# Kernel optimization log

Hardware: AMD Instinct MI355X
Metric: run time of the kernel (lower is better)

## Reference

```python
import jax, jax.numpy as jnp
import numpy as np

DIM = 768
HEADS = 12
HD = DIM // HEADS
SCALE = float(np.sqrt(HD))  # sqrt(dim // num_heads)


def layernorm(x, g, b, eps=1e-5):
    m = jnp.mean(x, axis=-1, keepdims=True)
    v = jnp.var(x, axis=-1, keepdims=True)
    return (x - m) * jax.lax.rsqrt(v + eps) * g + b


def dwconv(x, w, b, pad):
    # x: [B,C,H,W], w: [C,1,kh,kw] depthwise
    y = jax.lax.conv_general_dilated(
        x, w, window_strides=(1, 1), padding=[(pad, pad), (pad, pad)],
        feature_group_count=x.shape[1], dimension_numbers=('NCHW', 'OIHW', 'NCHW'))
    return y + b[None, :, None, None]


def mha(xq, xkv, wq, bq, wk, bk, wv, bv, wo, bo):
    # per-head Linears batched over heads; wq/wk/wv: [H, C, hd], biases [H, hd]
    B, N, C = xq.shape
    q = jnp.einsum('bnc,hcd->bhnd', xq, wq) + bq[None, :, None, :]
    k = jnp.einsum('bnc,hcd->bhnd', xkv, wk) + bk[None, :, None, :]
    v = jnp.einsum('bnc,hcd->bhnd', xkv, wv) + bv[None, :, None, :]
    z = jax.nn.sigmoid(jnp.einsum('bhnd,bhmd->bhnm', q, k) / SCALE)  # sigmoid, not softmax
    o = jnp.einsum('bhnm,bhmd->bhnd', z, v)
    o = o.transpose(0, 2, 1, 3).reshape(B, N, C)  # concat heads along feature dim
    return o @ wo + bo


def reference(decoder, wq1, bq1, wk1, bk1, wv1, bv1, wo1, bo1,
              wq2, bq2, wk2, bk2, wv2, bv2, wo2, bo2,
              alphas1, alphas2, peg_w, peg_b,
              ln1_g, ln1_b, ln2_g, ln2_b,
              cn_dw_w, cn_dw_b, cn_ln_g, cn_ln_b,
              cn_w1, cn_b1, cn_w2, cn_b2, cn_scale, cn_alphas):
    B, C, H, W = decoder.shape
    x = decoder.transpose(0, 2, 3, 1).reshape(B, H * W, C)  # [B,N,C]
    # block 1: alpha * x + MHA(x,x,x)
    x = alphas1 * x + mha(x, x, wq1, bq1, wk1, bk1, wv1, bv1, wo1, bo1)
    # PEG: depthwise 3x3 conv (replaces x, no residual in source)
    x4 = x.reshape(B, H, W, C).transpose(0, 3, 1, 2)
    x4 = dwconv(x4, peg_w, peg_b, pad=1)
    x = x4.transpose(0, 2, 3, 1).reshape(B, H * W, C)
    x = layernorm(x, ln1_g, ln1_b)
    # block 2 (encoder is None -> self-attention)
    x = alphas2 * x + mha(x, x, wq2, bq2, wk2, bk2, wv2, bv2, wo2, bo2)
    x = layernorm(x, ln2_g, ln2_b)
    x4 = x.reshape(B, H, W, C).transpose(0, 3, 1, 2)  # [B,C,H,W]
    # CNBlock head: dwconv7x7 -> LN -> Linear(4d) -> GELU -> Linear(d), layer_scale + alpha residual
    y = dwconv(x4, cn_dw_w, cn_dw_b, pad=3)
    y = y.transpose(0, 2, 3, 1)  # [B,H,W,C]
    y = layernorm(y, cn_ln_g, cn_ln_b)
    y = jax.nn.gelu(y @ cn_w1 + cn_b1, approximate=False)
    y = y @ cn_w2 + cn_b2
    y = y.transpose(0, 3, 1, 2)  # [B,C,H,W]
    out = cn_scale[None, :, None, None] * y + x4 * cn_alphas[None, :, None, None]
    return out


def setup_inputs() -> dict:
    key = jax.random.key(0)
    ks = iter(jax.random.split(key, 40))
    def n(shape, s=0.02):
        return jax.random.normal(next(ks), shape, dtype=jnp.float32) * s
    d = {}
    d['decoder'] = jax.random.normal(next(ks), (8, DIM, 32, 32), dtype=jnp.float32)
    for i in (1, 2):
        d[f'wq{i}'] = n((HEADS, DIM, HD)); d[f'bq{i}'] = n((HEADS, HD), 1e-6)
        d[f'wk{i}'] = n((HEADS, DIM, HD)); d[f'bk{i}'] = n((HEADS, HD), 1e-6)
        d[f'wv{i}'] = n((HEADS, DIM, HD)); d[f'bv{i}'] = n((HEADS, HD), 1e-6)
        d[f'wo{i}'] = n((DIM, DIM)); d[f'bo{i}'] = n((DIM,), 1e-6)
    d['alphas1'] = jnp.ones((DIM,), jnp.float32)
    d['alphas2'] = jnp.ones((DIM,), jnp.float32)
    d['peg_w'] = n((DIM, 1, 3, 3), 0.1); d['peg_b'] = n((DIM,), 1e-6)
    d['ln1_g'] = jnp.ones((DIM,), jnp.float32); d['ln1_b'] = jnp.zeros((DIM,), jnp.float32)
    d['ln2_g'] = jnp.ones((DIM,), jnp.float32); d['ln2_b'] = jnp.zeros((DIM,), jnp.float32)
    d['cn_dw_w'] = n((DIM, 1, 7, 7), 0.1); d['cn_dw_b'] = n((DIM,), 0.02)
    d['cn_ln_g'] = jnp.ones((DIM,), jnp.float32); d['cn_ln_b'] = jnp.zeros((DIM,), jnp.float32)
    d['cn_w1'] = n((DIM, 4 * DIM)); d['cn_b1'] = n((4 * DIM,), 0.02)
    d['cn_w2'] = n((4 * DIM, DIM)); d['cn_b2'] = n((DIM,), 0.02)
    d['cn_scale'] = jnp.full((DIM,), 1e-6, jnp.float32)
    d['cn_alphas'] = jnp.ones((DIM,), jnp.float32)
    return d
```

## Files before the change

### kernel.cpp

```cpp
#include <hip/hip_runtime.h>
#include <math.h>

#define BATCH 8
#define CDIM 768
#define NTOK 1024
#define NH 12
#define HDIM 64

typedef __attribute__((ext_vector_type(8))) short bf16x8;
typedef __attribute__((ext_vector_type(4))) float f32x4;

__device__ inline short f2bf(float f) {
    union { float f; unsigned u; } v; v.f = f;
    unsigned r = (v.u + 0x7FFF + ((v.u >> 16) & 1)) >> 16;
    return (short)r;
}

__device__ inline void async_copy16(const short* g, short* l) {
    __builtin_amdgcn_global_load_lds(
        (const __attribute__((address_space(1))) void*)g,
        (__attribute__((address_space(3))) void*)l, 16, 0, 0);
}

__global__ void k_transpose_in(const float* __restrict__ dec, float* __restrict__ x,
                               short* __restrict__ xb) {
    __shared__ float tile[32][33];
    int b = blockIdx.z;
    int n0 = blockIdx.x * 32;
    int c0 = blockIdx.y * 32;
    int tx = threadIdx.x, ty = threadIdx.y;
#pragma unroll
    for (int r = 0; r < 4; ++r) {
        int c = c0 + ty + r * 8;
        tile[ty + r * 8][tx] = dec[((size_t)b * CDIM + c) * NTOK + n0 + tx];
    }
    __syncthreads();
#pragma unroll
    for (int r = 0; r < 4; ++r) {
        int n = n0 + ty + r * 8;
        float val = tile[tx][ty + r * 8];
        size_t idx = ((size_t)b * NTOK + n) * CDIM + c0 + tx;
        x[idx] = val;
        xb[idx] = f2bf(val);
    }
}

__global__ void k_wtrans(const float* __restrict__ src, short* __restrict__ dst,
                         int R, int C) {
    __shared__ float tile[32][33];
    int c0 = blockIdx.x * 32, r0 = blockIdx.y * 32;
    int tx = threadIdx.x, ty = threadIdx.y;
#pragma unroll
    for (int p = 0; p < 4; ++p)
        tile[ty + p * 8][tx] = src[(size_t)(r0 + ty + p * 8) * C + c0 + tx];
    __syncthreads();
#pragma unroll
    for (int p = 0; p < 4; ++p)
        dst[(size_t)(c0 + ty + p * 8) * R + r0 + tx] = f2bf(tile[tx][ty + p * 8]);
}

__global__ __launch_bounds__(256) void k_packqkv(
    const float* __restrict__ wq1, const float* __restrict__ wk1, const float* __restrict__ wv1,
    const float* __restrict__ wq2, const float* __restrict__ wk2, const float* __restrict__ wv2,
    short* __restrict__ dst1, short* __restrict__ dst2) {
    __shared__ float tile[64][65];
    int z = blockIdx.y;
    int set = z / 36, rem = z % 36, sect = rem / 12, h = rem % 12;
    const float* srcs[6] = {wq1, wk1, wv1, wq2, wk2, wv2};
    const float* src = srcs[set * 3 + sect] + (size_t)h * 768 * 64;
    short* dst = (set ? dst2 : dst1) + ((size_t)sect * 768 + h * 64) * 768;
    int k0 = blockIdx.x * 64;
    int t = threadIdx.x;
#pragma unroll
    for (int p = 0; p < 16; ++p) {
        int gid = t + p * 256;
        int r = gid >> 6, c = gid & 63;
        tile[r][c] = src[(size_t)(k0 + r) * 64 + c];
    }
    __syncthreads();
#pragma unroll
    for (int p = 0; p < 16; ++p) {
        int gid = t + p * 256;
        int d = gid >> 6, kk = gid & 63;
        dst[(size_t)d * 768 + k0 + kk] = f2bf(tile[kk][d]);
    }
}

__global__ void k_packbias(const float* __restrict__ bq1, const float* __restrict__ bk1,
                           const float* __restrict__ bv1, const float* __restrict__ bq2,
                           const float* __restrict__ bk2, const float* __restrict__ bv2,
                           float* __restrict__ d1, float* __restrict__ d2) {
    int tid = blockIdx.x * 256 + threadIdx.x;
    if (tid >= 4608) return;
    int set = tid / 2304, n = tid % 2304;
    int sect = n / 768, rem = n % 768;
    const float* srcs[6] = {bq1, bk1, bv1, bq2, bk2, bv2};
    float v = srcs[set * 3 + sect][rem];
    (set ? d2 : d1)[n] = v;
}

#define GM_FINAL 0
#define GM_PROJ  1
#define GM_GELU  2
#define GM_QKV   3
#define QKVSEC ((size_t)BATCH * NH * NTOK * HDIM)

template<int MODE, int BN>
__global__ __launch_bounds__(256) void k_gemm_mfma(
    const short* __restrict__ A, const short* __restrict__ Bt,
    const float* __restrict__ bias, const float* __restrict__ resid,
    const float* __restrict__ rscale, const float* __restrict__ alph,
    float* __restrict__ outF, short* __restrict__ outB, int M, int N, int K) {
    constexpr int NT = BN / 32;
    constexpr int BP = BN / 64;
    constexpr int STAGE = 2 * 128 * 32 + 2 * BN * 32;
    constexpr int FINALS = (MODE == GM_FINAL) ? 64 * 132 * 2 : 0;
    constexpr int SMEM = STAGE > FINALS ? STAGE : FINALS;
    __shared__ short smem[SMEM];
    short* As = smem;
    short* Bs = smem + 2 * 128 * 32;
    int t = threadIdx.x;
    int w = t >> 6, lane = t & 63, l15 = lane & 15, quad = lane >> 4;
    int r0 = blockIdx.x * 128, n0 = blockIdx.y * BN;
    int wr = (w >> 1) * 64, wc = (w & 1) * (BN / 2);
    f32x4 acc[4][NT];
#pragma unroll
    for (int i = 0; i < 4; ++i)
#pragma unroll
        for (int j = 0; j < NT; ++j) acc[i][j] = (f32x4){0.f, 0.f, 0.f, 0.f};
    int sr = t >> 2, sc = (t & 3) * 8;
    const short* Ag = A + (size_t)(r0 + sr) * K + sc;
    const short* Bg = Bt + (size_t)(n0 + sr) * K + sc;
    short* AsW = As + w * 512;
    short* BsW = Bs + w * 512;
#pragma unroll
    for (int p = 0; p < 2; ++p)
        async_copy16(Ag, AsW + p * 2048), Ag += (size_t)64 * K * 0;
#pragma unroll
    for (int p = 0; p < 2; ++p)
        ;
#pragma unroll
    for (int p = 0; p < 2; ++p)
        async_copy16(Ag + (size_t)p * 64 * K, AsW + p * 2048);
#pragma unroll
    for (int p = 0; p < BP; ++p)
        async_copy16(Bg + (size_t)p * 64 * K, BsW + p * 2048);
    int st = 0;
    for (int k0 = 0; k0 < K; k0 += 32, st ^= 1) {
        __syncthreads();
        if (k0 + 32 < K) {
            int nst = st ^ 1;
#pragma unroll
            for (int p = 0; p < 2; ++p)
                async_copy16(Ag + k0 + 32 + (size_t)p * 64 * K,
                             AsW + nst * 4096 + p * 2048);
#pragma unroll
            for (int p = 0; p < BP; ++p)
                async_copy16(Bg + k0 + 32 + (size_t)p * 64 * K,
                             BsW + nst * (BN * 32) + p * 2048);
        }
        bf16x8 af[4], bf[NT];
#pragma unroll
        for (int i = 0; i < 4; ++i)
            af[i] = *(const bf16x8*)&As[st * 4096 + (wr + i * 16 + l15) * 32 + quad * 8];
#pragma unroll
        for (int j = 0; j < NT; ++j)
            bf[j] = *(const bf16x8*)&Bs[st * (BN * 32) + (wc + j * 16 + l15) * 32 + quad * 8];
#pragma unroll
        for (int i = 0; i < 4; ++i)
#pragma unroll
            for (int j = 0; j < NT; ++j)
                acc[i][j] = __builtin_amdgcn_mfma_f32_16x16x32_bf16(af[i], bf[j], acc[i][j], 0, 0, 0);
    }
    if (MODE == GM_FINAL) {
        __syncthreads();
        float* T = (float*)smem;
#pragma unroll
        for (int i = 0; i < 4; ++i)
#pragma unroll
            for (int j = 0; j < NT; ++j)
#pragma unroll
                for (int rr = 0; rr < 4; ++rr) {
                    int rl = wr + i * 16 + quad * 4 + rr;
                    int cl = wc + j * 16 + l15;
                    int row = r0 + rl, col = n0 + cl;
                    float val = acc[i][j][rr] + bias[col];
                    val = rscale[col] * val + alph[col] * resid[(size_t)row * N + col];
                    T[cl * 132 + rl] = val;
                }
        __syncthreads();
        int c = t >> 2, qo = (t & 3) * 32;
        int b = r0 >> 10, tokbase = r0 & 1023;
        float* obase = outF + ((size_t)(b * 768 + n0 + c)) * 1024 + tokbase + qo;
#pragma unroll
        for (int ii = 0; ii < 8; ++ii)
            *(float4*)&obase[ii * 4] = *(float4*)&T[c * 132 + qo + ii * 4];
        return;
    }
#pragma unroll
    for (int i = 0; i < 4; ++i)
#pragma unroll
        for (int j = 0; j < NT; ++j)
#pragma unroll
            for (int rr = 0; rr < 4; ++rr) {
                int row = r0 + wr + i * 16 + quad * 4 + rr;
                int col = n0 + wc + j * 16 + l15;
                float val = acc[i][j][rr] + bias[col];
                if (MODE == GM_PROJ) {
                    val += rscale[col] * resid[(size_t)row * N + col];
                    outF[(size_t)row * N + col] = val;
                } else if (MODE == GM_GELU) {
                    float u = val * (1.0f + 0.044715f * val * val);
                    float zz = __builtin_amdgcn_rcpf(
                        1.0f + __builtin_amdgcn_exp2f(-2.3022082f * u));
                    outB[(size_t)row * N + col] = f2bf(val * zz);
                } else {
                    int sect = col / 768, rem = col - sect * 768;
                    int hh = rem >> 6, d = rem & 63;
                    int bb = row >> 10, tok = row & 1023;
                    outB[(size_t)sect * QKVSEC +
                         (((size_t)bb * NH + hh) * NTOK + tok) * HDIM + d] = f2bf(val);
                }
            }
}

__global__ __launch_bounds__(256) void k_attn_mfma(
    const short* __restrict__ q, const short* __restrict__ k,
    const short* __restrict__ v, short* __restrict__ o) {
    __shared__ short Ks[64][72];
    __shared__ short Vt[64][72];
    __shared__ short Ps[128][72];
    int b = blockIdx.z, h = blockIdx.y;
    int q0 = blockIdx.x * 128;
    int t = threadIdx.x;
    int w = t >> 6, lane = t & 63, l15 = lane & 15, quad = lane >> 4;
    size_t base = ((size_t)(b * NH + h)) * NTOK * HDIM;
    const short* qp = q + base;
    const short* kp = k + base;
    const short* vp = v + base;
    bf16x8 qf[2][2];
#pragma unroll
    for (int mt = 0; mt < 2; ++mt)
#pragma unroll
        for (int kc = 0; kc < 2; ++kc)
            qf[mt][kc] = *(const bf16x8*)&qp[(size_t)(q0 + w * 32 + mt * 16 + l15) * HDIM + kc * 32 + quad * 8];
    f32x4 oacc[2][4];
#pragma unroll
    for (int mt = 0; mt < 2; ++mt)
#pragma unroll
        for (int dt = 0; dt < 4; ++dt) oacc[mt][dt] = (f32x4){0.f, 0.f, 0.f, 0.f};
    for (int kt = 0; kt < 16; ++kt) {
        __syncthreads();
#pragma unroll
        for (int p = 0; p < 2; ++p) {
            int gid = t + p * 256;
            int r = gid >> 3, c8 = (gid & 7) * 8;
            *(bf16x8*)&Ks[r][c8] = *(const bf16x8*)&kp[(size_t)(kt * 64 + r) * HDIM + c8];
        }
#pragma unroll
        for (int p = 0; p < 2; ++p) {
            int tok = t & 63, d0 = (t >> 6) * 8 + p * 32;
            bf16x8 vv = *(const bf16x8*)&vp[(size_t)(kt * 64 + tok) * HDIM + d0];
#pragma unroll
            for (int j = 0; j < 8; ++j) Vt[d0 + j][tok] = vv[j];
        }
        __syncthreads();
        f32x4 sacc[2][4];
#pragma unroll
        for (int mt = 0; mt < 2; ++mt)
#pragma unroll
            for (int nt = 0; nt < 4; ++nt) sacc[mt][nt] = (f32x4){0.f, 0.f, 0.f, 0.f};
#pragma unroll
        for (int nt = 0; nt < 4; ++nt) {
            bf16x8 kf0 = *(const bf16x8*)&Ks[nt * 16 + l15][quad * 8];
            bf16x8 kf1 = *(const bf16x8*)&Ks[nt * 16 + l15][32 + quad * 8];
#pragma unroll
            for (int mt = 0; mt < 2; ++mt) {
                sacc[mt][nt] = __builtin_amdgcn_mfma_f32_16x16x32_bf16(qf[mt][0], kf0, sacc[mt][nt], 0, 0, 0);
                sacc[mt][nt] = __builtin_amdgcn_mfma_f32_16x16x32_bf16(qf[mt][1], kf1, sacc[mt][nt], 0, 0, 0);
            }
        }
#pragma unroll
        for (int mt = 0; mt < 2; ++mt)
#pragma unroll
            for (int nt = 0; nt < 4; ++nt)
#pragma unroll
                for (int rr = 0; rr < 4; ++rr) {
                    float s = sacc[mt][nt][rr];
                    float z = __builtin_amdgcn_rcpf(
                        1.0f + __builtin_amdgcn_exp2f(s * -0.18033688011112042f));
                    Ps[w * 32 + mt * 16 + quad * 4 + rr][nt * 16 + l15] = f2bf(z);
                }
        __syncthreads();
        bf16x8 vfr[2][4];
#pragma unroll
        for (int kc = 0; kc < 2; ++kc)
#pragma unroll
            for (int dt = 0; dt < 4; ++dt)
                vfr[kc][dt] = *(const bf16x8*)&Vt[dt * 16 + l15][kc * 32 + quad * 8];
#pragma unroll
        for (int mt = 0; mt < 2; ++mt)
#pragma unroll
            for (int kc = 0; kc < 2; ++kc) {
                bf16x8 pf = *(const bf16x8*)&Ps[w * 32 + mt * 16 + l15][kc * 32 + quad * 8];
#pragma unroll
                for (int dt = 0; dt < 4; ++dt)
                    oacc[mt][dt] = __builtin_amdgcn_mfma_f32_16x16x32_bf16(pf, vfr[kc][dt], oacc[mt][dt], 0, 0, 0);
            }
    }
#pragma unroll
    for (int mt = 0; mt < 2; ++mt)
#pragma unroll
        for (int dt = 0; dt < 4; ++dt)
#pragma unroll
            for (int rr = 0; rr < 4; ++rr) {
                int tok = q0 + w * 32 + mt * 16 + quad * 4 + rr;
                int c = h * 64 + dt * 16 + l15;
                o[((size_t)b * NTOK + tok) * CDIM + c] = f2bf(oacc[mt][dt][rr]);
            }
}

template<int K>
__global__ __launch_bounds__(256) void k_dwconv_t(
    const float* __restrict__ in, const float* __restrict__ w,
    const float* __restrict__ bias, float* __restrict__ out) {
    constexpr int PAD = K / 2;
    constexpr int KK = K * K;
    int t = threadIdx.x;
    int c = blockIdx.y * 64 + (t & 63);
    int j = blockIdx.x * 4 + (t >> 6);
    int b = blockIdx.z;
    float wr[KK];
#pragma unroll
    for (int qq = 0; qq < KK; ++qq) wr[qq] = w[(size_t)c * KK + qq];
    float bsv = bias[c];
    const float* base = in + (size_t)b * NTOK * CDIM + c;
    float win[K][K];
#pragma unroll
    for (int s = 1; s < K; ++s) {
        int ii = s - 1 - PAD;
#pragma unroll
        for (int qq = 0; qq < K; ++qq) {
            int jj = j - PAD + qq;
            win[s][qq] = (ii >= 0 && jj >= 0 && jj < 32)
                         ? base[(size_t)(ii * 32 + jj) * CDIM] : 0.0f;
        }
    }
#pragma unroll
    for (int i = 0; i < 32; ++i) {
#pragma unroll
        for (int r = 0; r < K - 1; ++r)
#pragma unroll
            for (int qq = 0; qq < K; ++qq) win[r][qq] = win[r + 1][qq];
        int ii = i + PAD;
#pragma unroll
        for (int qq = 0; qq < K; ++qq) {
            int jj = j - PAD + qq;
            win[K - 1][qq] = (ii < 32 && jj >= 0 && jj < 32)
                             ? base[(size_t)(ii * 32 + jj) * CDIM] : 0.0f;
        }
        float acc = bsv;
#pragma unroll
        for (int r = 0; r < K; ++r)
#pragma unroll
            for (int qq = 0; qq < K; ++qq)
                acc = fmaf(win[r][qq], wr[r * K + qq], acc);
        out[((size_t)b * NTOK + i * 32 + j) * CDIM + c] = acc;
    }
}

__global__ __launch_bounds__(256) void k_ln(
    const float* __restrict__ in, const float* __restrict__ g,
    const float* __restrict__ b, float* __restrict__ outF, short* __restrict__ outB) {
    int row = blockIdx.x;
    const float* xr = in + (size_t)row * CDIM;
    int t = threadIdx.x;
    float x0 = xr[t], x1 = xr[t + 256], x2 = xr[t + 512];
    float s = x0 + x1 + x2;
    float sq = x0 * x0 + x1 * x1 + x2 * x2;
#pragma unroll
    for (int off = 32; off > 0; off >>= 1) {
        s += __shfl_down(s, off);
        sq += __shfl_down(sq, off);
    }
    __shared__ float ws[4], wq2[4];
    int wid = t >> 6, lane = t & 63;
    if (lane == 0) { ws[wid] = s; wq2[wid] = sq; }
    __syncthreads();
    if (t == 0) {
        float S = ws[0] + ws[1] + ws[2] + ws[3];
        float Q = wq2[0] + wq2[1] + wq2[2] + wq2[3];
        float m = S * (1.0f / CDIM);
        float var = Q * (1.0f / CDIM) - m * m;
        ws[0] = m;
        wq2[0] = rsqrtf(var + 1e-5f);
    }
    __syncthreads();
    float m = ws[0], inv = wq2[0];
    float y0 = (x0 - m) * inv * g[t] + b[t];
    float y1 = (x1 - m) * inv * g[t + 256] + b[t + 256];
    float y2 = (x2 - m) * inv * g[t + 512] + b[t + 512];
    if (outF) {
        float* orow = outF + (size_t)row * CDIM;
        orow[t] = y0; orow[t + 256] = y1; orow[t + 512] = y2;
    }
    if (outB) {
        short* orow = outB + (size_t)row * CDIM;
        orow[t] = f2bf(y0); orow[t + 256] = f2bf(y1); orow[t + 512] = f2bf(y2);
    }
}

extern "C" void kernel_launch(void* const* d_in, const int* in_sizes, int n_in,
                              void* d_out, int out_size, void* d_ws, size_t ws_size,
                              hipStream_t stream) {
    const float* dec = (const float*)d_in[0];
    const float* wq1 = (const float*)d_in[1]; const float* bq1 = (const float*)d_in[2];
    const float* wk1 = (const float*)d_in[3]; const float* bk1 = (const float*)d_in[4];
    const float* wv1 = (const float*)d_in[5]; const float* bv1 = (const float*)d_in[6];
    const float* wo1 = (const float*)d_in[7]; const float* bo1 = (const float*)d_in[8];
    const float* wq2 = (const float*)d_in[9]; const float* bq2 = (const float*)d_in[10];
    const float* wk2 = (const float*)d_in[11]; const float* bk2 = (const float*)d_in[12];
    const float* wv2 = (const float*)d_in[13]; const float* bv2 = (const float*)d_in[14];
    const float* wo2 = (const float*)d_in[15]; const float* bo2 = (const float*)d_in[16];
    const float* alphas1 = (const float*)d_in[17];
    const float* alphas2 = (const float*)d_in[18];
    const float* peg_w = (const float*)d_in[19]; const float* peg_b = (const float*)d_in[20];
    const float* ln1_g = (const float*)d_in[21]; const float* ln1_b = (const float*)d_in[22];
    const float* ln2_g = (const float*)d_in[23]; const float* ln2_b = (const float*)d_in[24];
    const float* cn_dw_w = (const float*)d_in[25]; const float* cn_dw_b = (const float*)d_in[26];
    const float* cn_ln_g = (const float*)d_in[27]; const float* cn_ln_b = (const float*)d_in[28];
    const float* cn_w1 = (const float*)d_in[29]; const float* cn_b1 = (const float*)d_in[30];
    const float* cn_w2 = (const float*)d_in[31]; const float* cn_b2 = (const float*)d_in[32];
    const float* cn_scale = (const float*)d_in[33]; const float* cn_alphas = (const float*)d_in[34];
    float* out = (float*)d_out;

    const size_t S = (size_t)BATCH * NTOK * CDIM;
    float* A0 = (float*)d_ws;
    float* A1 = A0 + S;
    short* Xb  = (short*)(A1 + S);
    short* QKV = Xb + S;
    short* Ob  = QKV + 3 * S;
    short* Hb  = Ob + S;
    short* Wqkv1 = Hb + 2 * S;
    short* Wqkv2 = Wqkv1 + 2304 * 768;
    short* WoT1  = Wqkv2 + 2304 * 768;
    short* WoT2  = WoT1 + 768 * 768;
    short* W1T   = WoT2 + 768 * 768;
    short* W2T   = W1T + (size_t)3072 * 768;
    float* bqkv1 = (float*)(W2T + (size_t)768 * 3072);
    float* bqkv2 = bqkv1 + 2304;
    short* Hfull = QKV + 2 * S;

    dim3 tb(32, 8);
    dim3 dwgrid(8, 12, 8);

    k_packqkv<<<dim3(12, 72), 256, 0, stream>>>(wq1, wk1, wv1, wq2, wk2, wv2, Wqkv1, Wqkv2);
    k_wtrans<<<dim3(24, 24), tb, 0, stream>>>(wo1, WoT1, 768, 768);
    k_wtrans<<<dim3(24, 24), tb, 0, stream>>>(wo2, WoT2, 768, 768);
    k_wtrans<<<dim3(96, 24), tb, 0, stream>>>(cn_w1, W1T, 768, 3072);
    k_wtrans<<<dim3(24, 96), tb, 0, stream>>>(cn_w2, W2T, 3072, 768);
    k_packbias<<<18, 256, 0, stream>>>(bq1, bk1, bv1, bq2, bk2, bv2, bqkv1, bqkv2);

    k_transpose_in<<<dim3(32, 24, 8), tb, 0, stream>>>(dec, A0, Xb);

    k_gemm_mfma<GM_QKV, 128><<<dim3(64, 18), 256, 0, stream>>>(
        Xb, Wqkv1, bqkv1, nullptr, nullptr, nullptr, nullptr, QKV, 8192, 2304, 768);
    k_attn_mfma<<<dim3(8, 12, 8), 256, 0, stream>>>(QKV, QKV + S, QKV + 2 * S, Ob);
    k_gemm_mfma<GM_PROJ, 64><<<dim3(64, 12), 256, 0, stream>>>(
        Ob, WoT1, bo1, A0, alphas1, nullptr, A1, nullptr, 8192, 768, 768);
    k_dwconv_t<3><<<dwgrid, 256, 0, stream>>>(A1, peg_w, peg_b, A0);
    k_ln<<<8192, 256, 0, stream>>>(A0, ln1_g, ln1_b, A1, Xb);

    k_gemm_mfma<GM_QKV, 128><<<dim3(64, 18), 256, 0, stream>>>(
        Xb, Wqkv2, bqkv2, nullptr, nullptr, nullptr, nullptr, QKV, 8192, 2304, 768);
    k_attn_mfma<<<dim3(8, 12, 8), 256, 0, stream>>>(QKV, QKV + S, QKV + 2 * S, Ob);
    k_gemm_mfma<GM_PROJ, 64><<<dim3(64, 12), 256, 0, stream>>>(
        Ob, WoT2, bo2, A1, alphas2, nullptr, A0, nullptr, 8192, 768, 768);
    k_ln<<<8192, 256, 0, stream>>>(A0, ln2_g, ln2_b, A1, nullptr);

    k_dwconv_t<7><<<dwgrid, 256, 0, stream>>>(A1, cn_dw_w, cn_dw_b, A0);
    k_ln<<<8192, 256, 0, stream>>>(A0, cn_ln_g, cn_ln_b, nullptr, Xb);
    k_gemm_mfma<GM_GELU, 128><<<dim3(64, 24), 256, 0, stream>>>(
        Xb, W1T, cn_b1, nullptr, nullptr, nullptr, nullptr, Hfull, 8192, 3072, 768);
    k_gemm_mfma<GM_FINAL, 64><<<dim3(64, 12), 256, 0, stream>>>(
        Hfull, W2T, cn_b2, A1, cn_scale, cn_alphas, out, nullptr, 8192, 768, 3072);
}
```

Before: 619.4 us.

## Merge prep kernels into one launch and double-buffer the attention kernel

Seven weight-packing, bias-packing and input-transpose launches are folded into a single k_prep kernel that picks its task from the block index, which cuts launch overhead. The attention kernel now double-buffers K (async copied into a swizzled LDS layout) and V, swaps the MFMA operand order, writes P and the output as packed bf16 pairs, raises wave priority around the MFMA loops, and remaps blocks so that one XCD handles a contiguous set of heads. It also drops a stray duplicate async copy in the GEMM prologue. The cost is more LDS per attention block, a launch-bounds occupancy hint, and more complex control flow.

Result: faster. 578.6 us (-6.6%).

```diff
diff --git a/kernel.cpp b/kernel.cpp
--- a/kernel.cpp
+++ b/kernel.cpp
@@ -16,87 +16,95 @@
     return (short)r;
 }
 
+__device__ inline unsigned pack2bf(float lo, float hi) {
+    return (unsigned)(unsigned short)f2bf(lo) | ((unsigned)(unsigned short)f2bf(hi) << 16);
+}
+
 __device__ inline void async_copy16(const short* g, short* l) {
     __builtin_amdgcn_global_load_lds(
         (const __attribute__((address_space(1))) void*)g,
         (__attribute__((address_space(3))) void*)l, 16, 0, 0);
 }
 
-__global__ void k_transpose_in(const float* __restrict__ dec, float* __restrict__ x,
-                               short* __restrict__ xb) {
-    __shared__ float tile[32][33];
-    int b = blockIdx.z;
-    int n0 = blockIdx.x * 32;
-    int c0 = blockIdx.y * 32;
-    int tx = threadIdx.x, ty = threadIdx.y;
-#pragma unroll
-    for (int r = 0; r < 4; ++r) {
-        int c = c0 + ty + r * 8;
-        tile[ty + r * 8][tx] = dec[((size_t)b * CDIM + c) * NTOK + n0 + tx];
-    }
-    __syncthreads();
-#pragma unroll
-    for (int r = 0; r < 4; ++r) {
-        int n = n0 + ty + r * 8;
-        float val = tile[tx][ty + r * 8];
-        size_t idx = ((size_t)b * NTOK + n) * CDIM + c0 + tx;
-        x[idx] = val;
-        xb[idx] = f2bf(val);
-    }
-}
-
-__global__ void k_wtrans(const float* __restrict__ src, short* __restrict__ dst,
-                         int R, int C) {
-    __shared__ float tile[32][33];
-    int c0 = blockIdx.x * 32, r0 = blockIdx.y * 32;
-    int tx = threadIdx.x, ty = threadIdx.y;
-#pragma unroll
-    for (int p = 0; p < 4; ++p)
-        tile[ty + p * 8][tx] = src[(size_t)(r0 + ty + p * 8) * C + c0 + tx];
-    __syncthreads();
-#pragma unroll
-    for (int p = 0; p < 4; ++p)
-        dst[(size_t)(c0 + ty + p * 8) * R + r0 + tx] = f2bf(tile[tx][ty + p * 8]);
-}
-
-__global__ __launch_bounds__(256) void k_packqkv(
+__global__ __launch_bounds__(256) void k_prep(
     const float* __restrict__ wq1, const float* __restrict__ wk1, const float* __restrict__ wv1,
     const float* __restrict__ wq2, const float* __restrict__ wk2, const float* __restrict__ wv2,
-    short* __restrict__ dst1, short* __restrict__ dst2) {
-    __shared__ float tile[64][65];
-    int z = blockIdx.y;
-    int set = z / 36, rem = z % 36, sect = rem / 12, h = rem % 12;
-    const float* srcs[6] = {wq1, wk1, wv1, wq2, wk2, wv2};
-    const float* src = srcs[set * 3 + sect] + (size_t)h * 768 * 64;
-    short* dst = (set ? dst2 : dst1) + ((size_t)sect * 768 + h * 64) * 768;
-    int k0 = blockIdx.x * 64;
+    const float* __restrict__ wo1, const float* __restrict__ wo2,
+    const float* __restrict__ cnw1, const float* __restrict__ cnw2,
+    const float* __restrict__ bq1, const float* __restrict__ bk1, const float* __restrict__ bv1,
+    const float* __restrict__ bq2, const float* __restrict__ bk2, const float* __restrict__ bv2,
+    const float* __restrict__ dec,
+    short* __restrict__ Wqkv1, short* __restrict__ Wqkv2,
+    short* __restrict__ WoT1, short* __restrict__ WoT2,
+    short* __restrict__ W1T, short* __restrict__ W2T,
+    float* __restrict__ bqkv1, float* __restrict__ bqkv2,
+    float* __restrict__ A0, short* __restrict__ Xb) {
+    __shared__ float sh[64 * 65];
+    int bid = blockIdx.x;
     int t = threadIdx.x;
-#pragma unroll
-    for (int p = 0; p < 16; ++p) {
-        int gid = t + p * 256;
-        int r = gid >> 6, c = gid & 63;
-        tile[r][c] = src[(size_t)(k0 + r) * 64 + c];
-    }
-    __syncthreads();
-#pragma unroll
-    for (int p = 0; p < 16; ++p) {
-        int gid = t + p * 256;
-        int d = gid >> 6, kk = gid & 63;
-        dst[(size_t)d * 768 + k0 + kk] = f2bf(tile[kk][d]);
-    }
-}
-
-__global__ void k_packbias(const float* __restrict__ bq1, const float* __restrict__ bk1,
-                           const float* __restrict__ bv1, const float* __restrict__ bq2,
-                           const float* __restrict__ bk2, const float* __restrict__ bv2,
-                           float* __restrict__ d1, float* __restrict__ d2) {
-    int tid = blockIdx.x * 256 + threadIdx.x;
-    if (tid >= 4608) return;
-    int set = tid / 2304, n = tid % 2304;
-    int sect = n / 768, rem = n % 768;
-    const float* srcs[6] = {bq1, bk1, bv1, bq2, bk2, bv2};
-    float v = srcs[set * 3 + sect][rem];
-    (set ? d2 : d1)[n] = v;
+    if (bid < 864) {
+        int bx = bid % 12, z = bid / 12;
+        int set = z / 36, rem = z % 36, sect = rem / 12, hh = rem % 12;
+        const float* srcs[6] = {wq1, wk1, wv1, wq2, wk2, wv2};
+        const float* src = srcs[set * 3 + sect] + (size_t)hh * 768 * 64;
+        short* dst = (set ? Wqkv2 : Wqkv1) + ((size_t)sect * 768 + hh * 64) * 768;
+        int k0 = bx * 64;
+#pragma unroll
+        for (int p = 0; p < 16; ++p) {
+            int gid = t + p * 256;
+            int r = gid >> 6, c = gid & 63;
+            sh[r * 65 + c] = src[(size_t)(k0 + r) * 64 + c];
+        }
+        __syncthreads();
+#pragma unroll
+        for (int p = 0; p < 16; ++p) {
+            int gid = t + p * 256;
+            int d = gid >> 6, kk = gid & 63;
+            dst[(size_t)d * 768 + k0 + kk] = f2bf(sh[kk * 65 + d]);
+        }
+    } else if (bid < 6624) {
+        int r = bid - 864;
+        const float* src; short* dst; int R, C, bx, by;
+        if (r < 576)       { src = wo1;  dst = WoT1; R = 768;  C = 768;  bx = r % 24; by = r / 24; }
+        else if (r < 1152) { int s = r - 576;  src = wo2;  dst = WoT2; R = 768;  C = 768;  bx = s % 24; by = s / 24; }
+        else if (r < 3456) { int s = r - 1152; src = cnw1; dst = W1T;  R = 768;  C = 3072; bx = s % 96; by = s / 96; }
+        else               { int s = r - 3456; src = cnw2; dst = W2T;  R = 3072; C = 768;  bx = s % 24; by = s / 24; }
+        int c0 = bx * 32, r0 = by * 32, tx = t & 31, ty = t >> 5;
+#pragma unroll
+        for (int p = 0; p < 4; ++p)
+            sh[(ty + p * 8) * 33 + tx] = src[(size_t)(r0 + ty + p * 8) * C + c0 + tx];
+        __syncthreads();
+#pragma unroll
+        for (int p = 0; p < 4; ++p)
+            dst[(size_t)(c0 + ty + p * 8) * R + r0 + tx] = f2bf(sh[tx * 33 + ty + p * 8]);
+    } else if (bid < 6642) {
+        int tid = (bid - 6624) * 256 + t;
+        if (tid < 4608) {
+            int set = tid / 2304, n = tid % 2304;
+            int sect = n / 768, rem = n % 768;
+            const float* srcs[6] = {bq1, bk1, bv1, bq2, bk2, bv2};
+            float v = srcs[set * 3 + sect][rem];
+            (set ? bqkv2 : bqkv1)[n] = v;
+        }
+    } else {
+        int r = bid - 6642;
+        int bx = r % 32, by = (r / 32) % 24, bz = r / 768;
+        int n0 = bx * 32, c0 = by * 32, tx = t & 31, ty = t >> 5;
+#pragma unroll
+        for (int p = 0; p < 4; ++p) {
+            int c = c0 + ty + p * 8;
+            sh[(ty + p * 8) * 33 + tx] = dec[((size_t)bz * CDIM + c) * NTOK + n0 + tx];
+        }
+        __syncthreads();
+#pragma unroll
+        for (int p = 0; p < 4; ++p) {
+            int n = n0 + ty + p * 8;
+            float val = sh[tx * 33 + ty + p * 8];
+            size_t idx = ((size_t)bz * NTOK + n) * CDIM + c0 + tx;
+            A0[idx] = val;
+            Xb[idx] = f2bf(val);
+        }
+    }
 }
 
 #define GM_FINAL 0
@@ -133,12 +141,6 @@
     const short* Bg = Bt + (size_t)(n0 + sr) * K + sc;
     short* AsW = As + w * 512;
     short* BsW = Bs + w * 512;
-#pragma unroll
-    for (int p = 0; p < 2; ++p)
-        async_copy16(Ag, AsW + p * 2048), Ag += (size_t)64 * K * 0;
-#pragma unroll
-    for (int p = 0; p < 2; ++p)
-        ;
 #pragma unroll
     for (int p = 0; p < 2; ++p)
         async_copy16(Ag + (size_t)p * 64 * K, AsW + p * 2048);
@@ -224,100 +226,135 @@
             }
 }
 
-__global__ __launch_bounds__(256) void k_attn_mfma(
+__global__ __launch_bounds__(256, 3) void k_attn_mfma(
     const short* __restrict__ q, const short* __restrict__ k,
     const short* __restrict__ v, short* __restrict__ o) {
-    __shared__ short Ks[64][72];
-    __shared__ short Vt[64][72];
+    __shared__ short Ks[2][64 * 64];
+    __shared__ short Vt[2][64][72];
     __shared__ short Ps[128][72];
-    int b = blockIdx.z, h = blockIdx.y;
-    int q0 = blockIdx.x * 128;
     int t = threadIdx.x;
     int w = t >> 6, lane = t & 63, l15 = lane & 15, quad = lane >> 4;
+    int flat = blockIdx.x + (blockIdx.y << 3) + blockIdx.z * 96;
+    int xcd = flat & 7, slot = flat >> 3;
+    int qb = slot & 7, grp = xcd * 12 + (slot >> 3);
+    int h = grp % 12, b = grp / 12;
+    int q0 = qb * 128;
     size_t base = ((size_t)(b * NH + h)) * NTOK * HDIM;
     const short* qp = q + base;
     const short* kp = k + base;
     const short* vp = v + base;
+
     bf16x8 qf[2][2];
 #pragma unroll
-    for (int mt = 0; mt < 2; ++mt)
+    for (int nq = 0; nq < 2; ++nq)
 #pragma unroll
         for (int kc = 0; kc < 2; ++kc)
-            qf[mt][kc] = *(const bf16x8*)&qp[(size_t)(q0 + w * 32 + mt * 16 + l15) * HDIM + kc * 32 + quad * 8];
-    f32x4 oacc[2][4];
-#pragma unroll
-    for (int mt = 0; mt < 2; ++mt)
-#pragma unroll
-        for (int dt = 0; dt < 4; ++dt) oacc[mt][dt] = (f32x4){0.f, 0.f, 0.f, 0.f};
+            qf[nq][kc] = *(const bf16x8*)&qp[(size_t)(q0 + w * 32 + nq * 16 + l15) * HDIM + kc * 32 + quad * 8];
+
+    int r8 = lane >> 3;
+    const short* kg = kp + r8 * HDIM + (((lane & 7) ^ r8) << 3);
+    int vtok = t & 63, vd0 = (t >> 6) * 8;
+
+    f32x4 oacc[4][2];
+#pragma unroll
+    for (int dt = 0; dt < 4; ++dt)
+#pragma unroll
+        for (int nq = 0; nq < 2; ++nq) oacc[dt][nq] = (f32x4){0.f, 0.f, 0.f, 0.f};
+
+#pragma unroll
+    for (int p = 0; p < 2; ++p)
+        async_copy16(kg + (size_t)(p * 32 + w * 8) * HDIM, &Ks[0][(p * 32 + w * 8) * 64]);
+    {
+        bf16x8 v0 = *(const bf16x8*)&vp[(size_t)vtok * HDIM + vd0];
+        bf16x8 v1 = *(const bf16x8*)&vp[(size_t)vtok * HDIM + vd0 + 32];
+#pragma unroll
+        for (int j = 0; j < 8; ++j) {
+            Vt[0][vd0 + j][vtok] = v0[j];
+            Vt[0][vd0 + 32 + j][vtok] = v1[j];
+        }
+    }
+
+    short* prow0 = &Ps[w * 32 + l15][0];
+    short* prow1 = &Ps[w * 32 + 16 + l15][0];
+
     for (int kt = 0; kt < 16; ++kt) {
-        __syncthreads();
-#pragma unroll
-        for (int p = 0; p < 2; ++p) {
-            int gid = t + p * 256;
-            int r = gid >> 3, c8 = (gid & 7) * 8;
-            *(bf16x8*)&Ks[r][c8] = *(const bf16x8*)&kp[(size_t)(kt * 64 + r) * HDIM + c8];
-        }
-#pragma unroll
-        for (int p = 0; p < 2; ++p) {
-            int tok = t & 63, d0 = (t >> 6) * 8 + p * 32;
-            bf16x8 vv = *(const bf16x8*)&vp[(size_t)(kt * 64 + tok) * HDIM + d0];
-#pragma unroll
-            for (int j = 0; j < 8; ++j) Vt[d0 + j][tok] = vv[j];
-        }
-        __syncthreads();
-        f32x4 sacc[2][4];
-#pragma unroll
-        for (int mt = 0; mt < 2; ++mt)
-#pragma unroll
-            for (int nt = 0; nt < 4; ++nt) sacc[mt][nt] = (f32x4){0.f, 0.f, 0.f, 0.f};
-#pragma unroll
-        for (int nt = 0; nt < 4; ++nt) {
-            bf16x8 kf0 = *(const bf16x8*)&Ks[nt * 16 + l15][quad * 8];
-            bf16x8 kf1 = *(const bf16x8*)&Ks[nt * 16 + l15][32 + quad * 8];
-#pragma unroll
-            for (int mt = 0; mt < 2; ++mt) {
-                sacc[mt][nt] = __builtin_amdgcn_mfma_f32_16x16x32_bf16(qf[mt][0], kf0, sacc[mt][nt], 0, 0, 0);
-                sacc[mt][nt] = __builtin_amdgcn_mfma_f32_16x16x32_bf16(qf[mt][1], kf1, sacc[mt][nt], 0, 0, 0);
+        int cur = kt & 1, nxt = cur ^ 1;
+        __syncthreads();
+        bf16x8 vv0, vv1;
+        if (kt < 15) {
+            const short* kgn = kg + (size_t)((kt + 1) * 64) * HDIM;
+#pragma unroll
+            for (int p = 0; p < 2; ++p)
+                async_copy16(kgn + (size_t)(p * 32 + w * 8) * HDIM, &Ks[nxt][(p * 32 + w * 8) * 64]);
+            vv0 = *(const bf16x8*)&vp[((size_t)(kt + 1) * 64 + vtok) * HDIM + vd0];
+            vv1 = *(const bf16x8*)&vp[((size_t)(kt + 1) * 64 + vtok) * HDIM + vd0 + 32];
+        }
+        f32x4 sacc[4][2];
+#pragma unroll
+        for (int mk = 0; mk < 4; ++mk)
+#pragma unroll
+            for (int nq = 0; nq < 2; ++nq) sacc[mk][nq] = (f32x4){0.f, 0.f, 0.f, 0.f};
+        __builtin_amdgcn_s_setprio(1);
+#pragma unroll
+        for (int mk = 0; mk < 4; ++mk)
+#pragma unroll
+            for (int kc = 0; kc < 2; ++kc) {
+                bf16x8 kf = *(const bf16x8*)&Ks[cur][(mk * 16 + l15) * 64 + (((kc * 4 + quad) ^ (l15 & 7)) << 3)];
+#pragma unroll
+                for (int nq = 0; nq < 2; ++nq)
+                    sacc[mk][nq] = __builtin_amdgcn_mfma_f32_16x16x32_bf16(kf, qf[nq][kc], sacc[mk][nq], 0, 0, 0);
             }
-        }
-#pragma unroll
-        for (int mt = 0; mt < 2; ++mt)
-#pragma unroll
-            for (int nt = 0; nt < 4; ++nt)
-#pragma unroll
-                for (int rr = 0; rr < 4; ++rr) {
-                    float s = sacc[mt][nt][rr];
-                    float z = __builtin_amdgcn_rcpf(
-                        1.0f + __builtin_amdgcn_exp2f(s * -0.18033688011112042f));
-                    Ps[w * 32 + mt * 16 + quad * 4 + rr][nt * 16 + l15] = f2bf(z);
-                }
-        __syncthreads();
-        bf16x8 vfr[2][4];
+        __builtin_amdgcn_s_setprio(0);
+#pragma unroll
+        for (int mk = 0; mk < 4; ++mk)
+#pragma unroll
+            for (int nq = 0; nq < 2; ++nq) {
+                float z[4];
+#pragma unroll
+                for (int rr = 0; rr < 4; ++rr)
+                    z[rr] = __builtin_amdgcn_rcpf(
+                        1.0f + __builtin_amdgcn_exp2f(sacc[mk][nq][rr] * -0.18033688011112042f));
+                unsigned* pw = (unsigned*)((nq ? prow1 : prow0) + mk * 16 + quad * 4);
+                pw[0] = pack2bf(z[0], z[1]);
+                pw[1] = pack2bf(z[2], z[3]);
+            }
+        if (kt < 15) {
+#pragma unroll
+            for (int j = 0; j < 8; ++j) {
+                Vt[nxt][vd0 + j][vtok] = vv0[j];
+                Vt[nxt][vd0 + 32 + j][vtok] = vv1[j];
+            }
+        }
+        asm volatile("s_waitcnt lgkmcnt(0)" ::: "memory");
+        __builtin_amdgcn_sched_barrier(0);
+        bf16x8 pf[2][2];
 #pragma unroll
         for (int kc = 0; kc < 2; ++kc)
 #pragma unroll
-            for (int dt = 0; dt < 4; ++dt)
-                vfr[kc][dt] = *(const bf16x8*)&Vt[dt * 16 + l15][kc * 32 + quad * 8];
-#pragma unroll
-        for (int mt = 0; mt < 2; ++mt)
+            for (int nq = 0; nq < 2; ++nq)
+                pf[kc][nq] = *(const bf16x8*)((nq ? prow1 : prow0) + kc * 32 + quad * 8);
+        __builtin_amdgcn_s_setprio(1);
+#pragma unroll
+        for (int dt = 0; dt < 4; ++dt)
 #pragma unroll
             for (int kc = 0; kc < 2; ++kc) {
-                bf16x8 pf = *(const bf16x8*)&Ps[w * 32 + mt * 16 + l15][kc * 32 + quad * 8];
-#pragma unroll
-                for (int dt = 0; dt < 4; ++dt)
-                    oacc[mt][dt] = __builtin_amdgcn_mfma_f32_16x16x32_bf16(pf, vfr[kc][dt], oacc[mt][dt], 0, 0, 0);
+                bf16x8 vf = *(const bf16x8*)&Vt[cur][dt * 16 + l15][kc * 32 + quad * 8];
+#pragma unroll
+                for (int nq = 0; nq < 2; ++nq)
+                    oacc[dt][nq] = __builtin_amdgcn_mfma_f32_16x16x32_bf16(vf, pf[kc][nq], oacc[dt][nq], 0, 0, 0);
             }
-    }
-#pragma unroll
-    for (int mt = 0; mt < 2; ++mt)
-#pragma unroll
-        for (int dt = 0; dt < 4; ++dt)
-#pragma unroll
-            for (int rr = 0; rr < 4; ++rr) {
-                int tok = q0 + w * 32 + mt * 16 + quad * 4 + rr;
-                int c = h * 64 + dt * 16 + l15;
-                o[((size_t)b * NTOK + tok) * CDIM + c] = f2bf(oacc[mt][dt][rr]);
-            }
+        __builtin_amdgcn_s_setprio(0);
+    }
+#pragma unroll
+    for (int dt = 0; dt < 4; ++dt)
+#pragma unroll
+        for (int nq = 0; nq < 2; ++nq) {
+            int tok = q0 + w * 32 + nq * 16 + l15;
+            int c = h * 64 + dt * 16 + quad * 4;
+            unsigned* op = (unsigned*)&o[((size_t)b * NTOK + tok) * CDIM + c];
+            op[0] = pack2bf(oacc[dt][nq][0], oacc[dt][nq][1]);
+            op[1] = pack2bf(oacc[dt][nq][2], oacc[dt][nq][3]);
+        }
 }
 
 template<int K>
@@ -451,17 +488,12 @@
     float* bqkv2 = bqkv1 + 2304;
     short* Hfull = QKV + 2 * S;
 
-    dim3 tb(32, 8);
     dim3 dwgrid(8, 12, 8);
 
-    k_packqkv<<<dim3(12, 72), 256, 0, stream>>>(wq1, wk1, wv1, wq2, wk2, wv2, Wqkv1, Wqkv2);
-    k_wtrans<<<dim3(24, 24), tb, 0, stream>>>(wo1, WoT1, 768, 768);
-    k_wtrans<<<dim3(24, 24), tb, 0, stream>>>(wo2, WoT2, 768, 768);
-    k_wtrans<<<dim3(96, 24), tb, 0, stream>>>(cn_w1, W1T, 768, 3072);
-    k_wtrans<<<dim3(24, 96), tb, 0, stream>>>(cn_w2, W2T, 3072, 768);
-    k_packbias<<<18, 256, 0, stream>>>(bq1, bk1, bv1, bq2, bk2, bv2, bqkv1, bqkv2);
-
-    k_transpose_in<<<dim3(32, 24, 8), tb, 0, stream>>>(dec, A0, Xb);
+    k_prep<<<dim3(12786), 256, 0, stream>>>(
+        wq1, wk1, wv1, wq2, wk2, wv2, wo1, wo2, cn_w1, cn_w2,
+        bq1, bk1, bv1, bq2, bk2, bv2, dec,
+        Wqkv1, Wqkv2, WoT1, WoT2, W1T, W2T, bqkv1, bqkv2, A0, Xb);
 
     k_gemm_mfma<GM_QKV, 128><<<dim3(64, 18), 256, 0, stream>>>(
         Xb, Wqkv1, bqkv1, nullptr, nullptr, nullptr, nullptr, QKV, 8192, 2304, 768);
```
